# Performance work log

Hardware: AMD Instinct MI355X
Metric: run time of the kernel (lower is better)

Reference implementation:

```python
import jax, jax.numpy as jnp
import numpy as np

MS_KS = 9
C = 256
BN_EPS = 1e-5


def setup_inputs() -> dict:
    key = jax.random.key(0)
    k1, k2, k3 = jax.random.split(key, 3)
    p2_r = jax.random.normal(k1, (2, C, 64, 128), dtype=jnp.float32)
    conv_w = jax.random.normal(k2, (C, C, 1, MS_KS), dtype=jnp.float32) * 0.02
    conv1_w = jax.random.normal(k3, (1, C, 1, 1), dtype=jnp.float32) * 0.05
    bn_gamma = jnp.ones((1,), jnp.float32)
    bn_beta = jnp.zeros((1,), jnp.float32)
    return dict(p2_r=p2_r, conv_w=conv_w, conv1_w=conv1_w,
                bn_gamma=bn_gamma, bn_beta=bn_beta)


def _scnn_pass(x, M):
    # x: [b,c,h,w]. Each step applies conv(1,ms_ks) to a width-1 column with
    # zero padding ms_ks//2 -> only the center tap contributes, i.e. a 256x256
    # channel matmul per column, followed by relu and residual add.
    cols = jnp.moveaxis(x, 3, 0)  # [w,b,c,h]
    def step(carry, col):
        new = col + jax.nn.relu(jnp.einsum('oc,bch->boh', M, carry))
        return new, new
    _, outs = jax.lax.scan(step, cols[0], cols[1:])
    outs = jnp.concatenate([cols[:1], outs], axis=0)[::-1]  # mirrors out[::-1]
    return jnp.moveaxis(outs, 0, 3)


def _upsample_bilinear_ac(x, factor=4):
    # F.interpolate(mode='bilinear', align_corners=True)
    b, c, h, w = x.shape
    Ho, Wo = factor * h, factor * w
    ys = jnp.arange(Ho, dtype=x.dtype) * ((h - 1) / (Ho - 1))
    xs = jnp.arange(Wo, dtype=x.dtype) * ((w - 1) / (Wo - 1))
    y0 = jnp.floor(ys).astype(jnp.int32)
    y1 = jnp.minimum(y0 + 1, h - 1)
    wy = (ys - y0.astype(x.dtype))[None, None, :, None]
    rows = x[:, :, y0, :] * (1 - wy) + x[:, :, y1, :] * wy  # [b,c,Ho,w]
    x0 = jnp.floor(xs).astype(jnp.int32)
    x1 = jnp.minimum(x0 + 1, w - 1)
    wx = (xs - x0.astype(x.dtype))[None, None, None, :]
    return rows[:, :, :, x0] * (1 - wx) + rows[:, :, :, x1] * wx


def reference(p2_r, conv_w, conv1_w, bn_gamma, bn_beta):
    M = conv_w[:, :, 0, MS_KS // 2]  # center tap, [c_out, c_in]
    x = _scnn_pass(p2_r, M)                     # reverse=False
    x = _scnn_pass(x[:, :, :, ::-1], M)         # reverse=True (slices[::-1])
    x = _upsample_bilinear_ac(x, 4)             # [b,256,4h,4w]
    x = jnp.einsum('oc,bchw->bohw', conv1_w[:, :, 0, 0], x)  # 1x1 conv -> 1 ch
    # BatchNorm2d(1), training-mode batch statistics (biased variance)
    mean = jnp.mean(x, axis=(0, 2, 3), keepdims=True)
    var = jnp.mean((x - mean) ** 2, axis=(0, 2, 3), keepdims=True)
    x = (x - mean) * jax.lax.rsqrt(var + BN_EPS)
    x = x * bn_gamma[None, :, None, None] + bn_beta[None, :, None, None]
    return jax.nn.sigmoid(x)
```

## Files before the change

### kernel.cpp

```cpp
#include <hip/hip_runtime.h>


typedef _Float16 f16x8 __attribute__((ext_vector_type(8)));
typedef _Float16 f16x4 __attribute__((ext_vector_type(4)));
typedef float    f32x4 __attribute__((ext_vector_type(4)));

extern "C" __global__ void k_extract(const float* __restrict__ convw,
                                     _Float16* __restrict__ Md) {
  int q = blockIdx.x * 256 + threadIdx.x;
  float4 v = ((const float4*)convw)[q];
  float vv[4] = {v.x, v.y, v.z, v.w};
  int f = q * 4;
#pragma unroll
  for (int e = 0; e < 4; ++e) {
    int flat = f + e;
    if (flat % 9 == 4) Md[flat / 9] = (_Float16)vv[e];
  }
}

struct SM {
  _Float16 cy[2][256];
  _Float16 pad_[32];
  _Float16 cz[2][256];
  float    sp[128 * 32];
};

extern "C" __global__ void __launch_bounds__(512, 2)
k_scan(const float* __restrict__ p2, const _Float16* __restrict__ Md,
       const float* __restrict__ conv1, float* __restrict__ sout,
       float* __restrict__ stats) {
  __shared__ SM sm;
  const int tid  = threadIdx.x;
  const int l    = tid & 63;
  const int r    = tid >> 6;
  const int col  = l & 15;
  const int quad = l >> 4;
  const int b    = blockIdx.x >> 6;
  const int h    = blockIdx.x & 63;

  if (blockIdx.x == 0 && tid == 0) { stats[0] = 0.f; stats[1] = 0.f; }

  const bool isY = (col == 0);
  const bool isZ = (col == 1);

  const int m0 = (r * 2 + 0) * 16 + quad * 4;
  const int m1 = (r * 2 + 1) * 16 + quad * 4;

  f16x8 A0[8], A1[8];
#pragma unroll
  for (int ch = 0; ch < 8; ++ch) {
    A0[ch] = *(const f16x8*)(Md + ((r*2+0)*16 + col) * 256 + ch*32 + quad*8);
    A1[ch] = *(const f16x8*)(Md + ((r*2+1)*16 + col) * 256 + ch*32 + quad*8);
  }

  const float* pbase = p2 + (size_t)b * 2097152 + (size_t)h * 128;

  float vva[4], vvb[4];
  {
    float c0a[4], c0b[4];
    if (isY || isZ) {
#pragma unroll
      for (int i = 0; i < 4; ++i) {
        c0a[i] = pbase[(size_t)(m0 + i) * 8192];
        c0b[i] = pbase[(size_t)(m1 + i) * 8192];
      }
    }
    if (isY) {
      f16x4 pa, pb;
#pragma unroll
      for (int i = 0; i < 4; ++i) { pa[i] = (_Float16)c0a[i]; pb[i] = (_Float16)c0b[i]; }
      *(f16x4*)(sm.cy[0] + m0) = pa; *(f16x4*)(sm.cy[0] + m1) = pb;
      *(f16x4*)(sm.cz[0] + m0) = pa; *(f16x4*)(sm.cz[0] + m1) = pb;
    }
    if (isZ) {
#pragma unroll
      for (int i = 0; i < 4; ++i) { vva[i] = conv1[m0 + i]; vvb[i] = conv1[m1 + i]; }
      float p = 0.f;
#pragma unroll
      for (int i = 0; i < 4; ++i) p += vva[i] * c0a[i] + vvb[i] * c0b[i];
      sm.sp[0 * 32 + r * 4 + quad] = p;
    }
  }

  float cca[4], ccb[4], cna[4], cnb[4];
  if (isY) {
#pragma unroll
    for (int i = 0; i < 4; ++i) {
      cca[i] = pbase[(size_t)(m0 + i) * 8192 + 1];
      ccb[i] = pbase[(size_t)(m1 + i) * 8192 + 1];
      cna[i] = pbase[(size_t)(m0 + i) * 8192 + 2];
      cnb[i] = pbase[(size_t)(m1 + i) * 8192 + 2];
    }
  }
  __syncthreads();

  const _Float16* selA = ((l & 1) ? sm.cz[0] : sm.cy[0]) + quad * 8;
  const _Float16* selB = ((l & 1) ? sm.cz[1] : sm.cy[1]) + quad * 8;

#define STEP(W, SELP, WY, WZ, CA, CB)                                          \
  do {                                                                         \
    f16x8 B[8];                                                                \
    _Pragma("unroll")                                                          \
    for (int ch = 0; ch < 8; ++ch)                                             \
      B[ch] = *(const f16x8*)((SELP) + ch * 32);                               \
    f32x4 a00 = {0.f,0.f,0.f,0.f}, a01 = {0.f,0.f,0.f,0.f};                    \
    f32x4 a10 = {0.f,0.f,0.f,0.f}, a11 = {0.f,0.f,0.f,0.f};                    \
    _Pragma("unroll")                                                          \
    for (int ch = 0; ch < 4; ++ch) {                                           \
      a00 = __builtin_amdgcn_mfma_f32_16x16x32_f16(A0[ch],   B[ch],   a00,0,0,0);\
      a10 = __builtin_amdgcn_mfma_f32_16x16x32_f16(A1[ch],   B[ch],   a10,0,0,0);\
      a01 = __builtin_amdgcn_mfma_f32_16x16x32_f16(A0[ch+4], B[ch+4], a01,0,0,0);\
      a11 = __builtin_amdgcn_mfma_f32_16x16x32_f16(A1[ch+4], B[ch+4], a11,0,0,0);\
    }                                                                          \
    f32x4 acc0 = a00 + a01, acc1 = a10 + a11;                                  \
    f16x4 yh0 = {}, yh1 = {};                                                  \
    if (isY) {                                                                 \
      _Pragma("unroll")                                                        \
      for (int i = 0; i < 4; ++i) {                                            \
        yh0[i] = (_Float16)((CA)[i] + fmaxf(acc0[i], 0.f));                    \
        yh1[i] = (_Float16)((CB)[i] + fmaxf(acc1[i], 0.f));                    \
      }                                                                        \
      *(f16x4*)((WY) + m0) = yh0;                                              \
      *(f16x4*)((WY) + m1) = yh1;                                              \
      if ((W) + 2 < 128) {                                                     \
        _Pragma("unroll")                                                      \
        for (int i = 0; i < 4; ++i) {                                          \
          (CA)[i] = pbase[(size_t)(m0 + i) * 8192 + (W) + 2];                  \
          (CB)[i] = pbase[(size_t)(m1 + i) * 8192 + (W) + 2];                  \
        }                                                                      \
      }                                                                        \
    }                                                                          \
    int2 u0 = __builtin_bit_cast(int2, yh0), u1 = __builtin_bit_cast(int2, yh1);\
    u0.x = __shfl(u0.x, l & 62, 64); u0.y = __shfl(u0.y, l & 62, 64);          \
    u1.x = __shfl(u1.x, l & 62, 64); u1.y = __shfl(u1.y, l & 62, 64);          \
    f16x4 ys0 = __builtin_bit_cast(f16x4, u0), ys1 = __builtin_bit_cast(f16x4, u1);\
    if (isZ) {                                                                 \
      f16x4 zh0, zh1;                                                          \
      float p = 0.f;                                                           \
      _Pragma("unroll")                                                        \
      for (int i = 0; i < 4; ++i) {                                            \
        float z0 = (float)ys0[i] + fmaxf(acc0[i], 0.f);                        \
        float z1 = (float)ys1[i] + fmaxf(acc1[i], 0.f);                        \
        zh0[i] = (_Float16)z0; zh1[i] = (_Float16)z1;                          \
        p += vva[i] * z0 + vvb[i] * z1;                                        \
      }                                                                        \
      *(f16x4*)((WZ) + m0) = zh0;                                              \
      *(f16x4*)((WZ) + m1) = zh1;                                              \
      sm.sp[(W) * 32 + r * 4 + quad] = p;                                      \
    }                                                                          \
    __syncthreads();                                                           \
  } while (0)

#pragma unroll 1
  for (int w = 1; w < 127; w += 2) {
    STEP(w,     selA, sm.cy[1], sm.cz[1], cca, ccb);
    STEP(w + 1, selB, sm.cy[0], sm.cz[0], cna, cnb);
  }
  STEP(127, selA, sm.cy[1], sm.cz[1], cca, ccb);
#undef STEP

  if (tid < 128) {
    const float4* q = (const float4*)(sm.sp + tid * 32);
    float s = 0.f;
#pragma unroll
    for (int j = 0; j < 8; ++j) { float4 t4 = q[j]; s += t4.x + t4.y + t4.z + t4.w; }
    sout[(blockIdx.x << 7) + (127 - tid)] = s;
  }
}

static __device__ __forceinline__ float bilin(const float* __restrict__ s,
                                              int idx) {
  int bb  = idx >> 17;
  int rem = idx & 131071;
  int ho  = rem >> 9;
  int wo  = rem & 511;
  const float SY = 63.0f / 255.0f, SX = 127.0f / 511.0f;
  float fy = (float)ho * SY;
  int y0 = (int)fy; int y1 = min(y0 + 1, 63); float wy = fy - (float)y0;
  float fx = (float)wo * SX;
  int x0 = (int)fx; int x1 = min(x0 + 1, 127); float wx = fx - (float)x0;
  const float* sb = s + bb * 8192;
  float cA = sb[y0 * 128 + x0] * (1.f - wy) + sb[y1 * 128 + x0] * wy;
  float cB = sb[y0 * 128 + x1] * (1.f - wy) + sb[y1 * 128 + x1] * wy;
  return cA * (1.f - wx) + cB * wx;
}

extern "C" __global__ void k_stats(const float* __restrict__ s,
                                   float* __restrict__ stats) {
  int tid  = threadIdx.x;
  int base = blockIdx.x * 1024 + tid;
  float sum = 0.f, ssq = 0.f;
#pragma unroll
  for (int i = 0; i < 4; ++i) {
    float u = bilin(s, base + i * 256);
    sum += u; ssq += u * u;
  }
#pragma unroll
  for (int off = 32; off > 0; off >>= 1) {
    sum += __shfl_xor(sum, off, 64);
    ssq += __shfl_xor(ssq, off, 64);
  }
  __shared__ float ls[4], lq[4];
  int wv = tid >> 6;
  if ((tid & 63) == 0) { ls[wv] = sum; lq[wv] = ssq; }
  __syncthreads();
  if (tid == 0) {
    atomicAdd(&stats[0], ls[0] + ls[1] + ls[2] + ls[3]);
    atomicAdd(&stats[1], lq[0] + lq[1] + lq[2] + lq[3]);
  }
}

extern "C" __global__ void k_norm(const float* __restrict__ s,
                                  const float* __restrict__ stats,
                                  const float* __restrict__ gamma,
                                  const float* __restrict__ beta,
                                  float* __restrict__ out) {
  int tid  = threadIdx.x;
  int base = blockIdx.x * 1024 + tid;
  const float invN = 1.f / 262144.f;
  float mean  = stats[0] * invN;
  float var   = stats[1] * invN - mean * mean;
  float scale = rsqrtf(var + 1e-5f) * gamma[0];
  float bias  = beta[0] - mean * scale;
#pragma unroll
  for (int i = 0; i < 4; ++i) {
    int idx = base + i * 256;
    float u = bilin(s, idx);
    float x = u * scale + bias;
    out[idx] = 1.f / (1.f + __expf(-x));
  }
}

extern "C" void kernel_launch(void* const* d_in, const int* in_sizes, int n_in,
                              void* d_out, int out_size, void* d_ws, size_t ws_size,
                              hipStream_t stream) {
  const float* p2    = (const float*)d_in[0];
  const float* convw = (const float*)d_in[1];
  const float* conv1 = (const float*)d_in[2];
  const float* gamma = (const float*)d_in[3];
  const float* beta  = (const float*)d_in[4];
  float* out = (float*)d_out;

  char* ws = (char*)d_ws;
  float*    s     = (float*)ws;
  float*    stats = (float*)(ws + 65536);
  _Float16* Md    = (_Float16*)(ws + 65792);

  hipLaunchKernelGGL(k_extract, dim3(576), dim3(256), 0, stream, convw, Md);
  hipLaunchKernelGGL(k_scan,    dim3(128), dim3(512), 0, stream, p2, Md, conv1, s, stats);
  hipLaunchKernelGGL(k_stats,   dim3(256), dim3(256), 0, stream, s, stats);
  hipLaunchKernelGGL(k_norm,    dim3(256), dim3(256), 0, stream, s, stats, gamma, beta, out);
}
```

Baseline: 186.6 us.

## Store all z columns in LDS, defer conv1 dot, lighten per-step sync and shuffles

The serial scan step now keeps every z column in a 128x256 fp16 LDS history instead of ping-pong buffers, and computes the conv1 projection once after the loop in parallel across all threads. Per-step cross-lane shuffles become a DPP even-lane broadcast, and __syncthreads is replaced by an explicit lgkmcnt wait plus s_barrier. The aim is to cut latency on the critical serial chain of 127 dependent steps. In exchange the LDS footprint grows to about 64KB, which could limit the two-blocks-per-CU occupancy, and the post-loop reduction now reads fp16-rounded z instead of fp32.

```diff
diff --git a/kernel.cpp b/kernel.cpp
--- a/kernel.cpp
+++ b/kernel.cpp
@@ -4,6 +4,18 @@
 typedef _Float16 f16x8 __attribute__((ext_vector_type(8)));
 typedef _Float16 f16x4 __attribute__((ext_vector_type(4)));
 typedef float    f32x4 __attribute__((ext_vector_type(4)));
+
+static __device__ __forceinline__ void sync_lds() {
+  asm volatile("s_waitcnt lgkmcnt(0)" ::: "memory");
+  __builtin_amdgcn_s_barrier();
+  asm volatile("" ::: "memory");
+}
+
+static __device__ __forceinline__ float dpp_even(float v) {
+  int t = __builtin_bit_cast(int, v);
+  t = __builtin_amdgcn_update_dpp(t, t, 0xA0, 0xF, 0xF, false);
+  return __builtin_bit_cast(float, t);
+}
 
 extern "C" __global__ void k_extract(const float* __restrict__ convw,
                                      _Float16* __restrict__ Md) {
@@ -21,8 +33,7 @@
 struct SM {
   _Float16 cy[2][256];
   _Float16 pad_[32];
-  _Float16 cz[2][256];
-  float    sp[128 * 32];
+  _Float16 zh[128 * 256];
 };
 
 extern "C" __global__ void __launch_bounds__(512, 2)
@@ -40,8 +51,9 @@
 
   if (blockIdx.x == 0 && tid == 0) { stats[0] = 0.f; stats[1] = 0.f; }
 
-  const bool isY = (col == 0);
-  const bool isZ = (col == 1);
+  const bool isY   = (col == 0);
+  const bool isZ   = (col == 1);
+  const bool zlane = (l & 1);
 
   const int m0 = (r * 2 + 0) * 16 + quad * 4;
   const int m1 = (r * 2 + 1) * 16 + quad * 4;
@@ -55,31 +67,18 @@
 
   const float* pbase = p2 + (size_t)b * 2097152 + (size_t)h * 128;
 
-  float vva[4], vvb[4];
-  {
+  if (isY) {
     float c0a[4], c0b[4];
-    if (isY || isZ) {
-#pragma unroll
-      for (int i = 0; i < 4; ++i) {
-        c0a[i] = pbase[(size_t)(m0 + i) * 8192];
-        c0b[i] = pbase[(size_t)(m1 + i) * 8192];
-      }
+#pragma unroll
+    for (int i = 0; i < 4; ++i) {
+      c0a[i] = pbase[(size_t)(m0 + i) * 8192];
+      c0b[i] = pbase[(size_t)(m1 + i) * 8192];
     }
-    if (isY) {
-      f16x4 pa, pb;
-#pragma unroll
-      for (int i = 0; i < 4; ++i) { pa[i] = (_Float16)c0a[i]; pb[i] = (_Float16)c0b[i]; }
-      *(f16x4*)(sm.cy[0] + m0) = pa; *(f16x4*)(sm.cy[0] + m1) = pb;
-      *(f16x4*)(sm.cz[0] + m0) = pa; *(f16x4*)(sm.cz[0] + m1) = pb;
-    }
-    if (isZ) {
-#pragma unroll
-      for (int i = 0; i < 4; ++i) { vva[i] = conv1[m0 + i]; vvb[i] = conv1[m1 + i]; }
-      float p = 0.f;
-#pragma unroll
-      for (int i = 0; i < 4; ++i) p += vva[i] * c0a[i] + vvb[i] * c0b[i];
-      sm.sp[0 * 32 + r * 4 + quad] = p;
-    }
+    f16x4 pa, pb;
+#pragma unroll
+    for (int i = 0; i < 4; ++i) { pa[i] = (_Float16)c0a[i]; pb[i] = (_Float16)c0b[i]; }
+    *(f16x4*)(sm.cy[0] + m0) = pa; *(f16x4*)(sm.cy[0] + m1) = pb;
+    *(f16x4*)(sm.zh    + m0) = pa; *(f16x4*)(sm.zh    + m1) = pb;
   }
 
   float cca[4], ccb[4], cna[4], cnb[4];
@@ -92,17 +91,20 @@
       cnb[i] = pbase[(size_t)(m1 + i) * 8192 + 2];
     }
   }
-  __syncthreads();
-
-  const _Float16* selA = ((l & 1) ? sm.cz[0] : sm.cy[0]) + quad * 8;
-  const _Float16* selB = ((l & 1) ? sm.cz[1] : sm.cy[1]) + quad * 8;
-
-#define STEP(W, SELP, WY, WZ, CA, CB)                                          \
+  sync_lds();
+
+  const _Float16* pY0 = sm.cy[0] + quad * 8;
+  const _Float16* pY1 = sm.cy[1] + quad * 8;
+  const _Float16* zrd = sm.zh + quad * 8;
+  _Float16*       zwr = sm.zh + 256;
+
+#define STEP(W, PY, WY, CA, CB)                                                \
   do {                                                                         \
+    const _Float16* bsrc = zlane ? zrd : (PY);                                 \
     f16x8 B[8];                                                                \
     _Pragma("unroll")                                                          \
     for (int ch = 0; ch < 8; ++ch)                                             \
-      B[ch] = *(const f16x8*)((SELP) + ch * 32);                               \
+      B[ch] = *(const f16x8*)(bsrc + ch * 32);                                 \
     f32x4 a00 = {0.f,0.f,0.f,0.f}, a01 = {0.f,0.f,0.f,0.f};                    \
     f32x4 a10 = {0.f,0.f,0.f,0.f}, a11 = {0.f,0.f,0.f,0.f};                    \
     _Pragma("unroll")                                                          \
@@ -113,12 +115,14 @@
       a11 = __builtin_amdgcn_mfma_f32_16x16x32_f16(A1[ch+4], B[ch+4], a11,0,0,0);\
     }                                                                          \
     f32x4 acc0 = a00 + a01, acc1 = a10 + a11;                                  \
-    f16x4 yh0 = {}, yh1 = {};                                                  \
+    f32x4 yf0 = {}, yf1 = {};                                                  \
     if (isY) {                                                                 \
+      f16x4 yh0, yh1;                                                          \
       _Pragma("unroll")                                                        \
       for (int i = 0; i < 4; ++i) {                                            \
-        yh0[i] = (_Float16)((CA)[i] + fmaxf(acc0[i], 0.f));                    \
-        yh1[i] = (_Float16)((CB)[i] + fmaxf(acc1[i], 0.f));                    \
+        yf0[i] = (CA)[i] + fmaxf(acc0[i], 0.f);                                \
+        yf1[i] = (CB)[i] + fmaxf(acc1[i], 0.f);                                \
+        yh0[i] = (_Float16)yf0[i]; yh1[i] = (_Float16)yf1[i];                  \
       }                                                                        \
       *(f16x4*)((WY) + m0) = yh0;                                              \
       *(f16x4*)((WY) + m1) = yh1;                                              \
@@ -130,41 +134,52 @@
         }                                                                      \
       }                                                                        \
     }                                                                          \
-    int2 u0 = __builtin_bit_cast(int2, yh0), u1 = __builtin_bit_cast(int2, yh1);\
-    u0.x = __shfl(u0.x, l & 62, 64); u0.y = __shfl(u0.y, l & 62, 64);          \
-    u1.x = __shfl(u1.x, l & 62, 64); u1.y = __shfl(u1.y, l & 62, 64);          \
-    f16x4 ys0 = __builtin_bit_cast(f16x4, u0), ys1 = __builtin_bit_cast(f16x4, u1);\
+    _Pragma("unroll")                                                          \
+    for (int i = 0; i < 4; ++i) {                                              \
+      yf0[i] = dpp_even(yf0[i]);                                               \
+      yf1[i] = dpp_even(yf1[i]);                                               \
+    }                                                                          \
     if (isZ) {                                                                 \
       f16x4 zh0, zh1;                                                          \
-      float p = 0.f;                                                           \
       _Pragma("unroll")                                                        \
       for (int i = 0; i < 4; ++i) {                                            \
-        float z0 = (float)ys0[i] + fmaxf(acc0[i], 0.f);                        \
-        float z1 = (float)ys1[i] + fmaxf(acc1[i], 0.f);                        \
-        zh0[i] = (_Float16)z0; zh1[i] = (_Float16)z1;                          \
-        p += vva[i] * z0 + vvb[i] * z1;                                        \
+        zh0[i] = (_Float16)(yf0[i] + fmaxf(acc0[i], 0.f));                     \
+        zh1[i] = (_Float16)(yf1[i] + fmaxf(acc1[i], 0.f));                     \
       }                                                                        \
-      *(f16x4*)((WZ) + m0) = zh0;                                              \
-      *(f16x4*)((WZ) + m1) = zh1;                                              \
-      sm.sp[(W) * 32 + r * 4 + quad] = p;                                      \
-    }                                                                          \
-    __syncthreads();                                                           \
+      *(f16x4*)(zwr + m0) = zh0;                                               \
+      *(f16x4*)(zwr + m1) = zh1;                                               \
+    }                                                                          \
+    zrd += 256; zwr += 256;                                                    \
+    sync_lds();                                                                \
   } while (0)
 
 #pragma unroll 1
   for (int w = 1; w < 127; w += 2) {
-    STEP(w,     selA, sm.cy[1], sm.cz[1], cca, ccb);
-    STEP(w + 1, selB, sm.cy[0], sm.cz[0], cna, cnb);
-  }
-  STEP(127, selA, sm.cy[1], sm.cz[1], cca, ccb);
+    STEP(w,     pY0, sm.cy[1], cca, ccb);
+    STEP(w + 1, pY1, sm.cy[0], cna, cnb);
+  }
+  STEP(127, pY0, sm.cy[1], cca, ccb);
 #undef STEP
 
-  if (tid < 128) {
-    const float4* q = (const float4*)(sm.sp + tid * 32);
+  {
+    const int w    = tid >> 2;
+    const int part = tid & 3;
+    const _Float16* zr = sm.zh + w * 256 + part * 64;
+    const float*    vr = conv1 + part * 64;
     float s = 0.f;
 #pragma unroll
-    for (int j = 0; j < 8; ++j) { float4 t4 = q[j]; s += t4.x + t4.y + t4.z + t4.w; }
-    sout[(blockIdx.x << 7) + (127 - tid)] = s;
+    for (int j = 0; j < 8; ++j) {
+      f16x8 zv = *(const f16x8*)(zr + j * 8);
+      float4 v0 = *(const float4*)(vr + j * 8);
+      float4 v1 = *(const float4*)(vr + j * 8 + 4);
+      s += v0.x * (float)zv[0] + v0.y * (float)zv[1]
+         + v0.z * (float)zv[2] + v0.w * (float)zv[3]
+         + v1.x * (float)zv[4] + v1.y * (float)zv[5]
+         + v1.z * (float)zv[6] + v1.w * (float)zv[7];
+    }
+    s += __shfl_xor(s, 1, 64);
+    s += __shfl_xor(s, 2, 64);
+    if (part == 0) sout[(blockIdx.x << 7) + (127 - w)] = s;
   }
 }
 
```

Result: faster. 178.9 us (-4.1%).
